# Optimization experiments

Hardware: AMD Instinct MI355X
Metric: run time of the kernel (lower is better)

The kernel has to match this reference:

```python
import jax, jax.numpy as jnp
import numpy as np

GRID = (128, 128, 128)
CENTER = np.array([0.0, 0.0, 0.0], dtype=np.float32)
SIZE = np.array([214.0, 214.0, 214.0], dtype=np.float32)
N_LORS = 65536
_CRYSTAL = SIZE[2] / GRID[2]
KERNEL_WIDTH = float(np.sqrt(_CRYSTAL * _CRYSTAL / np.pi))  # TOR gaussian sigma


def _make_lors(key, n, s):
    # rows: x1, y1, z1, x2, y2, z2 ; main direction along the 3rd coordinate
    k1, k2 = jax.random.split(key)
    trans = jax.random.uniform(k1, (4, n), jnp.float32, -0.45 * s, 0.45 * s)
    jit = jax.random.uniform(k2, (2, n), jnp.float32, -0.02 * s, 0.02 * s)
    half = 0.5 * s
    return jnp.stack([trans[0], trans[1], -half + jit[0],
                      trans[2], trans[3], half + jit[1]]).astype(jnp.float32)


def _project_bp(lors, image, grid, center, size, sigma):
    """TOR (tube-of-response) projection + listmode backprojection.
    lors: [N,6]; image shape == grid; main ray axis = last grid axis.
    Returns (line_integrals [N], backprojection volume grid)."""
    n0, n1, n2 = grid
    center = jnp.asarray(center, jnp.float32)
    size = jnp.asarray(size, jnp.float32)
    vox = size / jnp.array(grid, jnp.float32)
    xmin = center[0] - 0.5 * size[0]
    ymin = center[1] - 0.5 * size[1]
    zmin = center[2] - 0.5 * size[2]
    p1, p2 = lors[:, 0:3], lors[:, 3:6]
    d = p2 - p1
    L = jnp.sqrt(jnp.sum(d * d, axis=1))                    # [N]
    dz = d[:, 2]
    dz = jnp.where(jnp.abs(dz) < 1e-6, 1e-6, dz)
    zc = zmin + (jnp.arange(n2, dtype=jnp.float32) + 0.5) * vox[2]  # [K]
    t = (zc[None, :] - p1[:, 2:3]) / dz[:, None]            # [N,K] ray param per slice
    xs = p1[:, 0:1] + t * d[:, 0:1]                         # [N,K]
    ys = p1[:, 1:2] + t * d[:, 1:2]
    fi = (xs - xmin) / vox[0] - 0.5
    fj = (ys - ymin) / vox[1] - 0.5
    i0 = jnp.round(fi).astype(jnp.int32)
    j0 = jnp.round(fj).astype(jnp.int32)
    off = jnp.arange(-1, 2, dtype=jnp.int32)                # 3x3 in-plane TOR window
    oi = jnp.repeat(off, 3)                                  # [9]
    oj = jnp.tile(off, 3)                                    # [9]
    ii = i0[..., None] + oi                                  # [N,K,9]
    jj = j0[..., None] + oj
    inb = ((ii >= 0) & (ii < n0) & (jj >= 0) & (jj < n1)
           & (t[..., None] >= 0.0) & (t[..., None] <= 1.0))
    iic = jnp.clip(ii, 0, n0 - 1)
    jjc = jnp.clip(jj, 0, n1 - 1)
    dxv = (xmin + (iic.astype(jnp.float32) + 0.5) * vox[0]) - xs[..., None]
    dyv = (ymin + (jjc.astype(jnp.float32) + 0.5) * vox[1]) - ys[..., None]
    w = jnp.exp(-(dxv * dxv + dyv * dyv) / (2.0 * sigma * sigma))
    w = jnp.where(inb, w, 0.0)                               # [N,K,9]
    dl = vox[2] * L / jnp.abs(dz)                            # path length per slice [N]
    kk = jnp.broadcast_to(jnp.arange(n2, dtype=jnp.int32)[None, :, None], ii.shape)
    vals = image[iic, jjc, kk]                               # gather [N,K,9]
    proj = jnp.sum(w * vals, axis=(1, 2)) * dl               # [N]
    # listmode MLEM backprojection of 1/projection along same TOR weights
    contrib = w * (dl / (proj + 1e-8))[:, None, None]        # [N,K,9]
    flat = (iic * n1 + jjc) * n2 + kk
    bp = jnp.zeros(n0 * n1 * n2, jnp.float32).at[flat.reshape(-1)].add(
        contrib.reshape(-1)).reshape(n0, n1, n2)
    return proj, bp


def setup_inputs() -> dict:
    key = jax.random.key(0)
    kimg, keff, kx, ky, kz = jax.random.split(key, 5)
    image = jax.random.uniform(kimg, GRID, jnp.float32, 0.5, 1.5)
    effmap = jax.random.uniform(keff, GRID, jnp.float32, 0.5, 1.5)
    s = float(SIZE[0])
    return {
        'image': image,
        'efficiency_map': effmap,
        'xlors': _make_lors(kx, N_LORS, s),
        'ylors': _make_lors(ky, N_LORS, s),
        'zlors': _make_lors(kz, N_LORS, s),
    }


def reference(image, efficiency_map, xlors, ylors, zlors):
    g0, g1, g2 = GRID
    sigma = KERNEL_WIDTH
    imgz = image
    imgx = jnp.transpose(imgz, (2, 0, 1))
    imgy = jnp.transpose(imgz, (1, 0, 2))
    # stored as [6, N] -> [N, 6]
    xl, yl, zl = xlors.T, ylors.T, zlors.T
    pz, bpz = _project_bp(zl, imgz, GRID, CENTER, SIZE, sigma)
    gridx = (g0, g2, g1)
    px, bpx = _project_bp(xl, imgx, gridx, CENTER[[0, 2, 1]], SIZE[[0, 2, 1]], sigma)
    bpxt = jnp.transpose(bpx, (1, 2, 0))
    gridy = (g1, g2, g0)
    py, bpy = _project_bp(yl, imgy, gridy, CENTER[[1, 2, 0]], SIZE[[1, 2, 0]], sigma)
    bpyt = jnp.transpose(bpy, (1, 0, 2))
    return imgz / (efficiency_map + 1e-8) * (bpxt + bpyt + bpz)
```

## Files before the change

kernel.cpp:

```cpp
#include <hip/hip_runtime.h>
#include <hip/hip_fp16.h>
#include <math.h>

#define NLOR  65536
#define NG    128
#define PLANE (NG * NG)
#define NSUB  2
#define KG    8
#define NKG   (NG / KG)

#define VOX    1.671875f
#define XMIN  (-107.0f)
#define C2     1.57079632679f
#define C2L    2.26618007f

#define INVFPSCALE (1.0f / 8388608.0f)

#define PLP    129

#define PRM_STRIDE 8

typedef _Float16 h2v __attribute__((ext_vector_type(2)));

#if defined(__has_builtin)
#if __has_builtin(__builtin_amdgcn_fdot2)
#define HAVE_FDOT2 1
#endif
#endif

__device__ __forceinline__ float fdot2w(unsigned w, h2v wt, float c)
{
#ifdef HAVE_FDOT2
    return __builtin_amdgcn_fdot2(__builtin_bit_cast(h2v, w), wt, c, false);
#else
    const __half2 h = *reinterpret_cast<const __half2*>(&w);
    const float2 f = __half22float2(h);
    return c + (float)wt.x * f.x + (float)wt.y * f.y;
#endif
}

template<int SP, int SQ, int SR, int CONTIG>
__device__ __forceinline__ void permute_half_body(
    const float* __restrict__ in, __half* __restrict__ out,
    int b, float (*tile)[33])
{
    const int c0 = blockIdx.x * 32;
    const int r0 = blockIdx.y * 32;
    const int tx = threadIdx.x, ty = threadIdx.y;

#pragma unroll
    for (int m = 0; m < 4; ++m) {
        const int C = c0 + tx;
        const int R = r0 + ty + 8 * m;
        const int P = (CONTIG == 0) ? C : b;
        const int Q = (CONTIG == 0) ? b : C;
        tile[ty + 8 * m][tx] = in[P * SP + Q * SQ + R * SR];
    }
    __syncthreads();
#pragma unroll
    for (int m = 0; m < 4; ++m) {
        const int R = r0 + tx;
        const int C = c0 + ty + 8 * m;
        const int P = (CONTIG == 0) ? C : b;
        const int Q = (CONTIG == 0) ? b : C;
        const int o = P * PLANE + Q * NG + R;
        out[o] = __float2half(tile[tx][ty + 8 * m]);
    }
}

__global__ __launch_bounds__(256)
void perm_img2(const float* __restrict__ image,
               __half* __restrict__ imgPz, __half* __restrict__ imgPx,
               const float* __restrict__ zl, const float* __restrict__ yl,
               const float* __restrict__ xl,
               float* __restrict__ prmz, float* __restrict__ prmy,
               float* __restrict__ prmx)
{
    __shared__ float tile[32][33];
    const int b = blockIdx.z;
    if (b < 128) {
        permute_half_body<1, 16384, 128, 0>(image, imgPz, b, tile);
        return;
    }
    if (b < 256) {
        permute_half_body<128, 1, 16384, 1>(image, imgPx, b - 128, tile);
        return;
    }
    const int linear = (b - 256) * 16 + blockIdx.y * 4 + blockIdx.x;
    const int gid = linear * 256 + threadIdx.y * 32 + threadIdx.x;
    const int f   = gid >> 16;
    const int lor = gid & (NLOR - 1);
    const float* lors = (f == 0) ? zl : (f == 1) ? yl : xl;
    float* prm        = (f == 0) ? prmz : (f == 1) ? prmy : prmx;

    const float p1x = lors[0 * NLOR + lor];
    const float p1y = lors[1 * NLOR + lor];
    const float p1z = lors[2 * NLOR + lor];
    const float dx  = lors[3 * NLOR + lor] - p1x;
    const float dy  = lors[4 * NLOR + lor] - p1y;
    float dz = lors[5 * NLOR + lor] - p1z;
    dz = (fabsf(dz) < 1e-6f) ? 1e-6f : dz;
    const float rdz = 1.0f / dz;

    const float zc0 = XMIN + 0.5f * VOX;
    const float t0 = (zc0 - p1z) * rdz;
    float u0 = (fmaf(t0, dx, p1x) - XMIN) * (1.0f / VOX) - 0.5f;
    float v0 = (fmaf(t0, dy, p1y) - XMIN) * (1.0f / VOX) - 0.5f;
    float du = dx * rdz;
    float dv = dy * rdz;
    if (f == 1) {
        float tmp = u0; u0 = v0; v0 = tmp;
        tmp = du; du = dv; dv = tmp;
    }
    const float ka = (p1z - zc0) * (1.0f / VOX);
    const float kb = ka + dz * (1.0f / VOX);
    const float klo = fminf(ka, kb);
    const float khi = fmaxf(ka, kb);

    float4* p4 = (float4*)(prm + (size_t)lor * PRM_STRIDE);
    p4[0] = make_float4(u0, du, v0, dv);
    p4[1] = make_float4(klo, khi, 0.0f, 0.0f);
}

template<int NS>
__device__ __forceinline__ void proj_body(
    const float* const* prmv, const unsigned int* __restrict__ imgP,
    float* const* p8v, unsigned int* pl)
{
    const int g     = blockIdx.x;
    const int chunk = blockIdx.y;
    const int tid   = threadIdx.x;
    const int lor0  = chunk * 2048 + tid;
    const float k0  = (float)(g * KG);

    float kloA[2 * NS], khiA[2 * NS], uA[2 * NS], vA[2 * NS],
          duA[2 * NS], dvA[2 * NS], sA[2 * NS];
#pragma unroll
    for (int s = 0; s < 2 * NS; ++s) {
        const float* prm = prmv[s >> 1];
        const int lor = lor0 + (s & 1) * 1024;
        const float4* p4 = (const float4*)(prm + (size_t)lor * PRM_STRIDE);
        const float4 a = p4[0];
        const float4 b = p4[1];
        kloA[s] = b.x - k0;  khiA[s] = b.y - k0;
        uA[s] = fmaf(k0, a.y, a.x);  duA[s] = a.y;
        vA[s] = fmaf(k0, a.w, a.z);  dvA[s] = a.w;
        sA[s] = 0.0f;
    }

    uint4 pf0, pf1;
    {
        const uint4* src = (const uint4*)(imgP + (g * KG) * (NG * 64));
        pf0 = src[tid];
        pf1 = src[tid + 1024];
    }

    for (int st = 0; st < KG; ++st) {
        __syncthreads();
        uint4* dst = (uint4*)pl;
        dst[tid]        = pf0;
        dst[tid + 1024] = pf1;
        __syncthreads();
        if (st + 1 < KG) {
            const uint4* src = (const uint4*)(imgP + (g * KG + st + 1) * (NG * 64));
            pf0 = src[tid];
            pf1 = src[tid + 1024];
        }

        const float fst = (float)st;
#pragma unroll
        for (int s = 0; s < 2 * NS; ++s) {
            const float u = fmaf(fst, duA[s], uA[s]);
            const float v = fmaf(fst, dvA[s], vA[s]);
            const float fi = rintf(u);
            const float fj = rintf(v);
            const int i0 = (int)fi;
            const int j0 = (int)fj;
            const float mi = fi - u;
            const float mj = fj - v;
            const float ci = -C2L * mi,  cj = -C2L * mj;
            const float a0i = ci * mi,   a0j = cj * mj;
            const float gi = ci + ci,    gj = cj + cj;
            const float ki = a0i - C2L,  kj = a0j - C2L;
            const float exm = __builtin_amdgcn_exp2f(ki - gi);
            const float ex0 = __builtin_amdgcn_exp2f(a0i);
            const float exq = __builtin_amdgcn_exp2f(ki + gi);
            const float eym = __builtin_amdgcn_exp2f(kj - gj);
            const float ey0 = __builtin_amdgcn_exp2f(a0j);
            const float eyq = __builtin_amdgcn_exp2f(kj + gj);

            const _Float16 hm = (_Float16)eym, h0 = (_Float16)ey0,
                           hq = (_Float16)eyq, hz = (_Float16)0.0f;
            const bool odd = (j0 & 1) != 0;
            h2v wLo, wHi;
            wLo.x = odd ? hm : hz;  wLo.y = odd ? h0 : hm;
            wHi.x = odd ? hq : h0;  wHi.y = odd ? hz : hq;

            const int w  = min(max((j0 - 1) >> 1, 0), 62);
            const int ib = min(max(i0 - 1, 0), 125);

            const float exv[3] = {exm, ex0, exq};
            float acc = 0.0f;
#pragma unroll
            for (int a = 0; a < 3; ++a) {
                const int rowb = (ib + a) << 6;
                const unsigned Aw = pl[rowb + w];
                const unsigned Bw = pl[rowb + w + 1];
                float rd = fdot2w(Bw, wHi, 0.0f);
                rd = fdot2w(Aw, wLo, rd);
                acc = fmaf(exv[a], rd, acc);
            }
            const bool tin = (fst >= kloA[s]) && (fst <= khiA[s]);
            sA[s] += tin ? acc : 0.0f;
        }
    }
#pragma unroll
    for (int s = 0; s < NS; ++s) {
        p8v[s][g * NLOR + lor0]        = sA[2 * s];
        p8v[s][g * NLOR + lor0 + 1024] = sA[2 * s + 1];
    }
}

__global__ __launch_bounds__(1024, 8)
void proj_all(const float* __restrict__ prmz, const float* __restrict__ prmy,
              const float* __restrict__ prmx,
              const unsigned int* __restrict__ imgPz, const unsigned int* __restrict__ imgPx,
              float* __restrict__ p8z, float* __restrict__ p8y,
              float* __restrict__ p8x)
{
    __shared__ unsigned int pl[NG * 64];
    if (blockIdx.z == 0) {
        const float* prmv[2] = {prmz, prmy};
        float* p8v[2] = {p8z, p8y};
        proj_body<2>(prmv, imgPz, p8v, pl);
    } else {
        const float* prmv[1] = {prmx};
        float* p8v[1] = {p8x};
        proj_body<1>(prmv, imgPx, p8v, pl);
    }
}

__global__ __launch_bounds__(256)
void reduce_cf3(const float* __restrict__ zl, const float* __restrict__ yl,
                const float* __restrict__ xl,
                const float* __restrict__ p8z, const float* __restrict__ p8y,
                const float* __restrict__ p8x,
                float* __restrict__ prmz, float* __restrict__ prmy,
                float* __restrict__ prmx)
{
    const int which = blockIdx.y;
    const float* lors  = (which == 0) ? zl  : (which == 1) ? yl  : xl;
    const float* part8 = (which == 0) ? p8z : (which == 1) ? p8y : p8x;
    float*       prm   = (which == 0) ? prmz : (which == 1) ? prmy : prmx;

    const int lor = blockIdx.x * 256 + threadIdx.x;
    float s = 0.0f;
#pragma unroll
    for (int g = 0; g < NKG; ++g) s += part8[g * NLOR + lor];

    const float p1x = lors[0 * NLOR + lor];
    const float p1y = lors[1 * NLOR + lor];
    const float p1z = lors[2 * NLOR + lor];
    const float dx  = lors[3 * NLOR + lor] - p1x;
    const float dy  = lors[4 * NLOR + lor] - p1y;
    const float dz0 = lors[5 * NLOR + lor] - p1z;
    const float L = sqrtf(dx * dx + dy * dy + dz0 * dz0);
    const float adz = fmaxf(fabsf(dz0), 1e-6f);
    const float dl = VOX * L / adz;
    const float cf = dl / (s * dl + 1e-8f);
    prm[(size_t)lor * PRM_STRIDE + 6] = __log2f(cf) + 23.0f;
}

__device__ __forceinline__ void bp_deposit(const float* __restrict__ prm,
    int lor, float fk, unsigned int* __restrict__ pl)
{
    const float4* p4 = (const float4*)(prm + (size_t)lor * PRM_STRIDE);
    const float4 a = p4[0];
    const float4 b = p4[1];
    const float u = fmaf(fk, a.y, a.x);
    const float v = fmaf(fk, a.w, a.z);
    const float fi = rintf(u);
    const float fj = rintf(v);
    const bool tin = (fk >= b.x) && (fk <= b.y);
    const float lcf = tin ? b.z : -1e30f;

    const float mi = fi - u;
    const float mj = fj - v;
    const float ci = -C2L * mi,  cj = -C2L * mj;
    const float a0i = fmaf(ci, mi, lcf);
    const float a0j = cj * mj;
    const float gi = ci + ci,    gj = cj + cj;
    const float ki = a0i - C2L,  kj = a0j - C2L;

    const float ex0 = __builtin_amdgcn_exp2f(a0i);
    const float exm = __builtin_amdgcn_exp2f(ki - gi);
    const float exq = __builtin_amdgcn_exp2f(ki + gi);
    const float ey0 = __builtin_amdgcn_exp2f(a0j);
    const float eym = __builtin_amdgcn_exp2f(kj - gj);
    const float eyq = __builtin_amdgcn_exp2f(kj + gj);

    const float fib = __builtin_amdgcn_fmed3f(fi, 1.0f, 126.0f);
    const float fjb = __builtin_amdgcn_fmed3f(fj, 1.0f, 126.0f);
    const int idx = (int)fmaf(fib, (float)PLP, fjb) - (PLP + 1);
    unsigned int* base = pl + idx;

    const float exv[3] = {exm, ex0, exq};
#pragma unroll
    for (int aa = 0; aa < 3; ++aa) {
        unsigned int* row = base + aa * PLP;
        atomicAdd(row + 0, (unsigned int)(exv[aa] * eym));
        atomicAdd(row + 1, (unsigned int)(exv[aa] * ey0));
        atomicAdd(row + 2, (unsigned int)(exv[aa] * eyq));
    }
}

__global__ __launch_bounds__(1024)
void bp_all(const float* __restrict__ prmz, const float* __restrict__ prmy,
            const float* __restrict__ prmx,
            float* __restrict__ bpA, float* __restrict__ bpB)
{
    __shared__ unsigned int pl[NG * PLP];
    const int k   = blockIdx.x >> 1;
    const int sub = blockIdx.x & 1;
    const int tid = threadIdx.x;

    for (int i = tid; i < NG * PLP; i += 1024) pl[i] = 0u;
    __syncthreads();

    const float fk = (float)k;
    const int lo = sub * (NLOR / NSUB);
    constexpr int NIT = (NLOR / NSUB) / 1024;
    float* bpsub;
    if (blockIdx.y == 0) {
#pragma unroll 2
        for (int it = 0; it < NIT; ++it) {
            const int lor = lo + tid + it * 1024;
            bp_deposit(prmz, lor, fk, pl);
            bp_deposit(prmy, lor, fk, pl);
        }
        bpsub = bpA;
    } else {
#pragma unroll 4
        for (int it = 0; it < NIT; ++it)
            bp_deposit(prmx, lo + tid + it * 1024, fk, pl);
        bpsub = bpB;
    }
    __syncthreads();

    float* dst = bpsub + ((size_t)(sub * NG + k)) * PLANE;
    for (int idx = tid; idx < PLANE; idx += 1024)
        dst[idx] = (float)pl[(idx & 127) * PLP + (idx >> 7)] * INVFPSCALE;
}

__global__ __launch_bounds__(256)
void finalize_out(const float* __restrict__ bpA, const float* __restrict__ bpB,
                  const float* __restrict__ img, const float* __restrict__ eff,
                  float* __restrict__ out)
{
    __shared__ float tA[32][33];
    const int b  = blockIdx.z;
    const int x0 = blockIdx.x * 32;
    const int z0 = blockIdx.y * 32;
    const int tx = threadIdx.x, ty = threadIdx.y;
    const int VOL = NG * PLANE;

#pragma unroll
    for (int m = 0; m < 4; ++m) {
        const int z = z0 + ty + 8 * m;
        const int a = z * PLANE + b * NG + (x0 + tx);
        tA[ty + 8 * m][tx] = bpA[a] + bpA[a + VOL];
    }
    __syncthreads();
#pragma unroll
    for (int m = 0; m < 4; ++m) {
        const int x  = x0 + ty + 8 * m;
        const int o  = x * PLANE + b * NG + (z0 + tx);
        const int bb = b * PLANE + x * NG + (z0 + tx);
        const float v = tA[tx][ty + 8 * m] + bpB[bb] + bpB[bb + VOL];
        out[o] = img[o] / (eff[o] + 1e-8f) * v;
    }
}

extern "C" void kernel_launch(void* const* d_in, const int* in_sizes, int n_in,
                              void* d_out, int out_size, void* d_ws, size_t ws_size,
                              hipStream_t stream) {
    const float* image = (const float*)d_in[0];
    const float* eff   = (const float*)d_in[1];
    const float* xl    = (const float*)d_in[2];
    const float* yl    = (const float*)d_in[3];
    const float* zl    = (const float*)d_in[4];
    float* out = (float*)d_out;

    char* ws = (char*)d_ws;
    __half* imgPz = (__half*)(ws);
    __half* imgPx = (__half*)(ws + (size_t)( 4 << 20));
    float* bpA    = (float*)(ws + (size_t)( 8 << 20));
    float* bpB    = (float*)(ws + (size_t)(24 << 20));
    float* p8z    = (float*)(ws + (size_t)(40 << 20));
    float* p8y    = (float*)(ws + (size_t)(44 << 20));
    float* p8x    = (float*)(ws + (size_t)(48 << 20));
    float* prmz   = (float*)(ws + (size_t)(52 << 20));
    float* prmy   = (float*)(ws + (size_t)(54 << 20));
    float* prmx   = (float*)(ws + (size_t)(56 << 20));

    const dim3 tb(32, 8);

    perm_img2<<<dim3(4, 4, 304), tb, 0, stream>>>(image, imgPz, imgPx,
        zl, yl, xl, prmz, prmy, prmx);
    proj_all<<<dim3(16, 32, 2), 1024, 0, stream>>>(prmz, prmy, prmx,
        (const unsigned int*)imgPz, (const unsigned int*)imgPx, p8z, p8y, p8x);
    reduce_cf3<<<dim3(256, 3), 256, 0, stream>>>(zl, yl, xl, p8z, p8y, p8x, prmz, prmy, prmx);
    bp_all<<<dim3(128 * NSUB, 2), 1024, 0, stream>>>(prmz, prmy, prmx, bpA, bpB);
    finalize_out<<<dim3(4, 4, 128), tb, 0, stream>>>(bpA, bpB, image, eff, out);
}
```

Baseline: 195.9 us.

## Bucket-sort LOR parameters by spatial key before backprojection to reduce atomic conflicts

Computes a per-LOR key from the ray's mid-volume in-plane position and scatters each LOR's parameter record into 32 interleaved buckets. Overflowing buckets are handled by a spill list and a new fixup kernel. The backprojection then reads the reordered parameters. Neighbouring threads now deposit into spread-out regions, which is meant to cut shared-memory atomic contention and bank conflicts in bp_all. The cost is an extra kernel launch, global atomics, and reusing workspace memory that the projection stage wrote earlier.

```diff
diff --git a/kernel.cpp b/kernel.cpp
--- a/kernel.cpp
+++ b/kernel.cpp
@@ -19,6 +19,9 @@
 #define PLP    129
 
 #define PRM_STRIDE 8
+
+#define NBKT   32
+#define SLOTS  (NLOR / NBKT)
 
 typedef _Float16 h2v __attribute__((ext_vector_type(2)));
 
@@ -74,7 +77,7 @@
                const float* __restrict__ zl, const float* __restrict__ yl,
                const float* __restrict__ xl,
                float* __restrict__ prmz, float* __restrict__ prmy,
-               float* __restrict__ prmx)
+               float* __restrict__ prmx, unsigned int* __restrict__ scb)
 {
     __shared__ float tile[32][33];
     const int b = blockIdx.z;
@@ -84,6 +87,13 @@
     }
     if (b < 256) {
         permute_half_body<128, 1, 16384, 1>(image, imgPx, b - 128, tile);
+        return;
+    }
+    if (b == 304) {
+        if (blockIdx.x == 0 && blockIdx.y == 0) {
+            const int t = threadIdx.y * 32 + threadIdx.x;
+            if (t < 102) scb[t] = 0u;
+        }
         return;
     }
     const int linear = (b - 256) * 16 + blockIdx.y * 4 + blockIdx.x;
@@ -117,9 +127,11 @@
     const float klo = fminf(ka, kb);
     const float khi = fmaxf(ka, kb);
 
+    const float key = rintf(fmaf(64.0f, du, u0)) + rintf(fmaf(64.0f, dv, v0));
+
     float4* p4 = (float4*)(prm + (size_t)lor * PRM_STRIDE);
     p4[0] = make_float4(u0, du, v0, dv);
-    p4[1] = make_float4(klo, khi, 0.0f, 0.0f);
+    p4[1] = make_float4(klo, khi, 0.0f, key);
 }
 
 template<int NS>
@@ -246,12 +258,15 @@
                 const float* __restrict__ p8z, const float* __restrict__ p8y,
                 const float* __restrict__ p8x,
                 float* __restrict__ prmz, float* __restrict__ prmy,
-                float* __restrict__ prmx)
+                float* __restrict__ prmx,
+                float* __restrict__ prmSz, float* __restrict__ prmSy,
+                float* __restrict__ prmSx, unsigned int* __restrict__ scb)
 {
     const int which = blockIdx.y;
     const float* lors  = (which == 0) ? zl  : (which == 1) ? yl  : xl;
     const float* part8 = (which == 0) ? p8z : (which == 1) ? p8y : p8x;
     float*       prm   = (which == 0) ? prmz : (which == 1) ? prmy : prmx;
+    float*       prmS  = (which == 0) ? prmSz : (which == 1) ? prmSy : prmSx;
 
     const int lor = blockIdx.x * 256 + threadIdx.x;
     float s = 0.0f;
@@ -268,7 +283,46 @@
     const float adz = fmaxf(fabsf(dz0), 1e-6f);
     const float dl = VOX * L / adz;
     const float cf = dl / (s * dl + 1e-8f);
-    prm[(size_t)lor * PRM_STRIDE + 6] = __log2f(cf) + 23.0f;
+
+    float4* p4 = (float4*)(prm + (size_t)lor * PRM_STRIDE);
+    const float4 a = p4[0];
+    float4 b = p4[1];
+    b.z = __log2f(cf) + 23.0f;
+    p4[1] = b;
+
+    const int bkt = ((int)b.w) & (NBKT - 1);
+    const unsigned r = atomicAdd(&scb[which * NBKT + bkt], 1u);
+    if (r < (unsigned)SLOTS) {
+        const int p = bkt + NBKT * (int)r;
+        float4* q = (float4*)(prmS + (size_t)p * PRM_STRIDE);
+        q[0] = a; q[1] = b;
+    } else {
+        const unsigned sp = atomicAdd(&scb[96 + which], 1u);
+        scb[128 + which * NLOR + sp] = (unsigned)lor;
+    }
+}
+
+__global__ __launch_bounds__(256)
+void fixup_scatter(const float* __restrict__ prmz, const float* __restrict__ prmy,
+                   const float* __restrict__ prmx,
+                   float* __restrict__ prmSz, float* __restrict__ prmSy,
+                   float* __restrict__ prmSx, unsigned int* __restrict__ scb)
+{
+    const int t = blockIdx.x * 256 + threadIdx.x;
+    const int f   = t >> 16;
+    const int rem = t & (NLOR - 1);
+    const int bkt = rem & (NBKT - 1);
+    const int r   = rem >> 5;
+    if ((unsigned)r < scb[f * NBKT + bkt]) return;
+
+    const unsigned sp = atomicAdd(&scb[99 + f], 1u);
+    const unsigned lorid = scb[128 + f * NLOR + sp];
+    const float* prm = (f == 0) ? prmz : (f == 1) ? prmy : prmx;
+    float* prmS      = (f == 0) ? prmSz : (f == 1) ? prmSy : prmSx;
+    const float4* src = (const float4*)(prm + (size_t)lorid * PRM_STRIDE);
+    float4* dst = (float4*)(prmS + (size_t)(bkt + NBKT * r) * PRM_STRIDE);
+    dst[0] = src[0];
+    dst[1] = src[1];
 }
 
 __device__ __forceinline__ void bp_deposit(const float* __restrict__ prm,
@@ -394,8 +448,12 @@
     char* ws = (char*)d_ws;
     __half* imgPz = (__half*)(ws);
     __half* imgPx = (__half*)(ws + (size_t)( 4 << 20));
+    float* prmSz  = (float*)(ws);
+    float* prmSy  = (float*)(ws + (size_t)( 2 << 20));
+    float* prmSx  = (float*)(ws + (size_t)( 4 << 20));
     float* bpA    = (float*)(ws + (size_t)( 8 << 20));
     float* bpB    = (float*)(ws + (size_t)(24 << 20));
+    unsigned int* scb = (unsigned int*)(ws + (size_t)(39 << 20));
     float* p8z    = (float*)(ws + (size_t)(40 << 20));
     float* p8y    = (float*)(ws + (size_t)(44 << 20));
     float* p8x    = (float*)(ws + (size_t)(48 << 20));
@@ -405,11 +463,14 @@
 
     const dim3 tb(32, 8);
 
-    perm_img2<<<dim3(4, 4, 304), tb, 0, stream>>>(image, imgPz, imgPx,
-        zl, yl, xl, prmz, prmy, prmx);
+    perm_img2<<<dim3(4, 4, 305), tb, 0, stream>>>(image, imgPz, imgPx,
+        zl, yl, xl, prmz, prmy, prmx, scb);
     proj_all<<<dim3(16, 32, 2), 1024, 0, stream>>>(prmz, prmy, prmx,
         (const unsigned int*)imgPz, (const unsigned int*)imgPx, p8z, p8y, p8x);
-    reduce_cf3<<<dim3(256, 3), 256, 0, stream>>>(zl, yl, xl, p8z, p8y, p8x, prmz, prmy, prmx);
-    bp_all<<<dim3(128 * NSUB, 2), 1024, 0, stream>>>(prmz, prmy, prmx, bpA, bpB);
+    reduce_cf3<<<dim3(256, 3), 256, 0, stream>>>(zl, yl, xl, p8z, p8y, p8x,
+        prmz, prmy, prmx, prmSz, prmSy, prmSx, scb);
+    fixup_scatter<<<dim3(768), 256, 0, stream>>>(prmz, prmy, prmx,
+        prmSz, prmSy, prmSx, scb);
+    bp_all<<<dim3(128 * NSUB, 2), 1024, 0, stream>>>(prmSz, prmSy, prmSx, bpA, bpB);
     finalize_out<<<dim3(4, 4, 128), tb, 0, stream>>>(bpA, bpB, image, eff, out);
 }
```

Measured after the change: 528.7 us. 170% more time.
